# Performance work log

Measured on AMD Instinct MI355X. Metric: run time of the kernel, lower is better.

The kernel has to match this reference:

```python
import jax, jax.numpy as jnp
import numpy as np

HIDDEN = 1024
D_MEM = 256
BATCH = 4
SEQ = 1024
EPS = 1e-6


def elu_plus_one(x):
    # F.elu(x) + 1 == exp(x) for x<0, x+1 for x>=0 (positive feature map)
    return jnp.where(x > 0, x + 1.0, jnp.exp(x))


def setup_inputs() -> dict:
    key = jax.random.key(0)
    ks = jax.random.split(key, 8)
    hidden_states = jax.random.normal(ks[0], (BATCH, SEQ, HIDDEN), dtype=jnp.float32)
    s = 1.0 / np.sqrt(HIDDEN)
    w_q = jax.random.normal(ks[1], (D_MEM, HIDDEN), dtype=jnp.float32) * s
    w_k = jax.random.normal(ks[2], (D_MEM, HIDDEN), dtype=jnp.float32) * s
    w_v = jax.random.normal(ks[3], (D_MEM, HIDDEN), dtype=jnp.float32) * s
    w_o = jax.random.normal(ks[4], (HIDDEN, D_MEM), dtype=jnp.float32) * (1.0 / np.sqrt(D_MEM))
    gate = jnp.zeros((1,), dtype=jnp.float32)
    # nonzero persistent memory state so retrieval path is exercised
    memory = jax.random.normal(ks[5], (D_MEM, D_MEM), dtype=jnp.float32) * 0.1
    memory_norm = jax.random.uniform(ks[6], (D_MEM,), dtype=jnp.float32) * 10.0 + 1.0
    return {
        "hidden_states": hidden_states,
        "w_q": w_q, "w_k": w_k, "w_v": w_v, "w_o": w_o,
        "gate": gate, "memory": memory, "memory_norm": memory_norm,
    }


def _retrieve(sigma_x, memory, memory_norm):
    # [b,s,d] @ [d,d] -> [b,s,d], normalized by sigma_x @ memory_norm
    a_unnorm = jnp.matmul(sigma_x, memory)
    norm = jnp.clip(jnp.matmul(sigma_x, memory_norm), EPS, None)[..., None]
    out = a_unnorm / norm
    # torch: if memory_norm.sum() < 1e-6 -> zeros
    return jnp.where(memory_norm.sum() < EPS, jnp.zeros_like(out), out)


def reference(hidden_states, w_q, w_k, w_v, w_o, gate, memory, memory_norm):
    b, s, _ = hidden_states.shape
    q = jnp.einsum('bsh,dh->bsd', hidden_states, w_q)
    k = jnp.einsum('bsh,dh->bsd', hidden_states, w_k)
    v = jnp.einsum('bsh,dh->bsd', hidden_states, w_v)

    sigma_q = elu_plus_one(q)
    sigma_k = elu_plus_one(k)

    # --- retrieval from compressive memory ---
    memory_output = _retrieve(sigma_q, memory, memory_norm)

    # --- causal linear attention within segment (cumsum form, as in source) ---
    kv = jnp.einsum('bsd,bse->bsde', sigma_k, v)          # [b,s,d,d]
    kv_cumsum = jnp.cumsum(kv, axis=1)                     # [b,s,d,d]
    k_cumsum = jnp.cumsum(sigma_k, axis=1)                 # [b,s,d]
    numerator = jnp.einsum('bsd,bsde->bse', sigma_q, kv_cumsum)
    denominator = jnp.clip(jnp.einsum('bsd,bsd->bs', sigma_q, k_cumsum), EPS, None)[..., None]
    local_output = numerator / denominator

    g = jax.nn.sigmoid(gate[0])
    combined = g * memory_output + (1.0 - g) * local_output
    output = jnp.einsum('bsd,hd->bsh', combined, w_o)

    # --- delta-rule memory update (detached in torch) ---
    retrieved_unnorm = jnp.matmul(sigma_k, memory)
    norm = jnp.clip(jnp.matmul(sigma_k, memory_norm), EPS, None)[..., None]
    delta_v = v - retrieved_unnorm / norm
    memory_update = jnp.einsum('bsd,bse->de', sigma_k, delta_v) / (b * s)
    new_memory = jax.lax.stop_gradient(memory + memory_update)
    z_update = sigma_k.sum(axis=(0, 1)) / b
    new_memory_norm = jax.lax.stop_gradient(memory_norm + z_update)

    return output, new_memory, new_memory_norm
```

## Files before the change

kernel.cpp:

```cpp
#include <hip/hip_runtime.h>


#define HIDDEN 1024
#define DMEM 256
#define BATCH 4
#define SEQ 1024
#define MTOT (BATCH * SEQ)
#define CHUNK 128
#define NCH (SEQ / CHUNK)
#define NCHT (BATCH * NCH)
#define EPSF 1e-6f

typedef __bf16 bf16x8 __attribute__((ext_vector_type(8)));
typedef __bf16 bf16x4 __attribute__((ext_vector_type(4)));
typedef float f32x4 __attribute__((ext_vector_type(4)));

#define GL_LDS(g, l)                                                                   \
  __builtin_amdgcn_global_load_lds((const __attribute__((address_space(1))) void*)(g), \
                                   (__attribute__((address_space(3))) void*)(l), 16, 0, 0)

__device__ __forceinline__ float elu1(float x) { return x > 0.f ? x + 1.f : __expf(x); }

__global__ void kprep(const float* __restrict__ hs, const float* __restrict__ wq,
                      const float* __restrict__ wk, const float* __restrict__ wv,
                      const float* __restrict__ wo, const float* __restrict__ mem,
                      __bf16* __restrict__ hsb, __bf16* __restrict__ wqkvb,
                      __bf16* __restrict__ wob, __bf16* __restrict__ memT,
                      float* __restrict__ out) {
  __shared__ float s[64][65];
  int b = blockIdx.x, tid = threadIdx.x;
  if (b < 4096) {
    int i = b * 256 + tid;
    float4 f = reinterpret_cast<const float4*>(hs)[i];
    bf16x4 h = {(__bf16)f.x, (__bf16)f.y, (__bf16)f.z, (__bf16)f.w};
    reinterpret_cast<bf16x4*>(hsb)[i] = h;
  } else if (b < 5120) {
    int y = (b - 4096) >> 8;
    const float* src = (y == 0) ? wq : (y == 1) ? wk : (y == 2) ? wv : wo;
    __bf16* dst = (y < 3) ? wqkvb + (size_t)y * (DMEM * HIDDEN) : wob;
    int i = ((b - 4096) & 255) * 256 + tid;
    float4 f = reinterpret_cast<const float4*>(src)[i];
    bf16x4 h = {(__bf16)f.x, (__bf16)f.y, (__bf16)f.z, (__bf16)f.w};
    reinterpret_cast<bf16x4*>(dst)[i] = h;
  } else if (b < 5136) {
    int t = b - 5120;
    int bx = t & 3, by = t >> 2;
    int r0 = tid >> 6, col = tid & 63;
#pragma unroll
    for (int it = 0; it < 16; ++it) {
      int row = it * 4 + r0;
      s[row][col] = mem[(size_t)(by * 64 + row) * DMEM + bx * 64 + col];
    }
    __syncthreads();
#pragma unroll
    for (int it = 0; it < 16; ++it) {
      int row = it * 4 + r0;
      memT[(size_t)(bx * 64 + row) * DMEM + by * 64 + col] = (__bf16)s[col][row];
    }
  } else {
    int g = (b - 5136) * 256 + tid;
    reinterpret_cast<float4*>(out + (size_t)MTOT * HIDDEN)[g] =
        reinterpret_cast<const float4*>(mem)[g];
  }
}

__global__ __launch_bounds__(256) void k1_qkv_mfma(
    const __bf16* __restrict__ X, const __bf16* __restrict__ W, __bf16* __restrict__ sqb,
    __bf16* __restrict__ skb, __bf16* __restrict__ skT, __bf16* __restrict__ vT) {
  __shared__ __bf16 As[128 * 32];
  __shared__ __bf16 Bs[128 * 32];
  int tid = threadIdx.x;
  int lane = tid & 63, wave = tid >> 6;
  int m0 = blockIdx.x * 128;
  int by = blockIdx.y;
  int wsel = by >> 1, n0 = (by & 1) * 128;
  const __bf16* aptr = X + (size_t)(m0 + (tid >> 2)) * HIDDEN + ((tid & 3) << 3);
  const __bf16* bptr = W + (size_t)(by * 128 + (tid >> 2)) * HIDDEN + ((tid & 3) << 3);
  int wr = wave >> 1, wc = wave & 1, quad = lane >> 4, l16 = lane & 15;
  f32x4 acc[4][4] = {};
  for (int k0 = 0; k0 < HIDDEN; k0 += 32) {
    GL_LDS(aptr + k0, As + wave * 512);
    GL_LDS(aptr + (size_t)64 * HIDDEN + k0, As + 2048 + wave * 512);
    GL_LDS(bptr + k0, Bs + wave * 512);
    GL_LDS(bptr + (size_t)64 * HIDDEN + k0, Bs + 2048 + wave * 512);
    __syncthreads();
    bf16x8 aF[4], bF[4];
#pragma unroll
    for (int i = 0; i < 4; ++i)
      aF[i] = *reinterpret_cast<const bf16x8*>(As + (wr * 64 + i * 16 + l16) * 32 + quad * 8);
#pragma unroll
    for (int j = 0; j < 4; ++j)
      bF[j] = *reinterpret_cast<const bf16x8*>(Bs + (wc * 64 + j * 16 + l16) * 32 + quad * 8);
#pragma unroll
    for (int i = 0; i < 4; ++i)
#pragma unroll
      for (int j = 0; j < 4; ++j)
        acc[i][j] = __builtin_amdgcn_mfma_f32_16x16x32_bf16(aF[i], bF[j], acc[i][j], 0, 0, 0);
    __syncthreads();
  }
#pragma unroll
  for (int i = 0; i < 4; ++i)
#pragma unroll
    for (int j = 0; j < 4; ++j) {
      int mb = m0 + wr * 64 + i * 16 + quad * 4;
      int n = n0 + wc * 64 + j * 16 + l16;
      if (wsel == 0) {
#pragma unroll
        for (int r = 0; r < 4; ++r) sqb[(size_t)(mb + r) * DMEM + n] = (__bf16)elu1(acc[i][j][r]);
      } else if (wsel == 1) {
        bf16x4 t;
#pragma unroll
        for (int r = 0; r < 4; ++r) {
          float v = elu1(acc[i][j][r]);
          skb[(size_t)(mb + r) * DMEM + n] = (__bf16)v;
          t[r] = (__bf16)v;
        }
        *reinterpret_cast<bf16x4*>(skT + (size_t)n * MTOT + mb) = t;
      } else {
        bf16x4 t;
#pragma unroll
        for (int r = 0; r < 4; ++r) t[r] = (__bf16)acc[i][j][r];
        *reinterpret_cast<bf16x4*>(vT + (size_t)n * MTOT + mb) = t;
      }
    }
}

__global__ __launch_bounds__(256) void kC(const __bf16* __restrict__ vT,
                                          const __bf16* __restrict__ skT,
                                          const __bf16* __restrict__ sqb,
                                          const __bf16* __restrict__ skb,
                                          __bf16* __restrict__ kvcT, __bf16* __restrict__ scb,
                                          float* __restrict__ ksc) {
  __shared__ __bf16 As[64 * 32];
  __shared__ __bf16 Bs[128 * 32];
  int tid = threadIdx.x;
  int c = blockIdx.x;
  int y = blockIdx.y;
  if (y == 10) {
    int d = tid;
    float s = 0.f;
    for (int i = 0; i < CHUNK; ++i) s += (float)skb[(size_t)(c * CHUNK + i) * DMEM + d];
    ksc[c * DMEM + d] = s;
    return;
  }
  int lane = tid & 63, wave = tid >> 6;
  int wr = wave >> 1, wc = wave & 1, quad = lane >> 4, l16 = lane & 15;
  if (y < 8) {
    int e0 = (y >> 1) * 64, d0 = (y & 1) * 128;
    const __bf16* aptr = vT + (size_t)(e0 + (tid >> 2)) * MTOT + c * CHUNK + ((tid & 3) << 3);
    const __bf16* bptr = skT + (size_t)(d0 + (tid >> 2)) * MTOT + c * CHUNK + ((tid & 3) << 3);
    f32x4 acc[2][4] = {};
    for (int k0 = 0; k0 < CHUNK; k0 += 32) {
      GL_LDS(aptr + k0, As + wave * 512);
      GL_LDS(bptr + k0, Bs + wave * 512);
      GL_LDS(bptr + (size_t)64 * MTOT + k0, Bs + 2048 + wave * 512);
      __syncthreads();
      bf16x8 aF[2], bF[4];
#pragma unroll
      for (int i = 0; i < 2; ++i)
        aF[i] = *reinterpret_cast<const bf16x8*>(As + (wr * 32 + i * 16 + l16) * 32 + quad * 8);
#pragma unroll
      for (int j = 0; j < 4; ++j)
        bF[j] = *reinterpret_cast<const bf16x8*>(Bs + (wc * 64 + j * 16 + l16) * 32 + quad * 8);
#pragma unroll
      for (int i = 0; i < 2; ++i)
#pragma unroll
        for (int j = 0; j < 4; ++j)
          acc[i][j] = __builtin_amdgcn_mfma_f32_16x16x32_bf16(aF[i], bF[j], acc[i][j], 0, 0, 0);
      __syncthreads();
    }
#pragma unroll
    for (int i = 0; i < 2; ++i)
#pragma unroll
      for (int j = 0; j < 4; ++j)
#pragma unroll
        for (int r = 0; r < 4; ++r) {
          int e = e0 + wr * 32 + i * 16 + quad * 4 + r;
          int d = d0 + wc * 64 + j * 16 + l16;
          kvcT[(size_t)c * DMEM * DMEM + (size_t)e * DMEM + d] = (__bf16)acc[i][j][r];
        }
  } else {
    int i0 = (y - 8) * 64;
    const __bf16* aptr =
        sqb + (size_t)(c * CHUNK + i0 + (tid >> 2)) * DMEM + ((tid & 3) << 3);
    const __bf16* bptr = skb + (size_t)(c * CHUNK + (tid >> 2)) * DMEM + ((tid & 3) << 3);
    f32x4 acc[2][4] = {};
    for (int k0 = 0; k0 < DMEM; k0 += 32) {
      GL_LDS(aptr + k0, As + wave * 512);
      GL_LDS(bptr + k0, Bs + wave * 512);
      GL_LDS(bptr + (size_t)64 * DMEM + k0, Bs + 2048 + wave * 512);
      __syncthreads();
      bf16x8 aF[2], bF[4];
#pragma unroll
      for (int i = 0; i < 2; ++i)
        aF[i] = *reinterpret_cast<const bf16x8*>(As + (wr * 32 + i * 16 + l16) * 32 + quad * 8);
#pragma unroll
      for (int j = 0; j < 4; ++j)
        bF[j] = *reinterpret_cast<const bf16x8*>(Bs + (wc * 64 + j * 16 + l16) * 32 + quad * 8);
#pragma unroll
      for (int i = 0; i < 2; ++i)
#pragma unroll
        for (int j = 0; j < 4; ++j)
          acc[i][j] = __builtin_amdgcn_mfma_f32_16x16x32_bf16(aF[i], bF[j], acc[i][j], 0, 0, 0);
      __syncthreads();
    }
#pragma unroll
    for (int i = 0; i < 2; ++i)
#pragma unroll
      for (int j = 0; j < 4; ++j)
#pragma unroll
        for (int r = 0; r < 4; ++r) {
          int ii = i0 + wr * 32 + i * 16 + quad * 4 + r;
          int jj = wc * 64 + j * 16 + l16;
          scb[(size_t)c * CHUNK * CHUNK + (size_t)ii * CHUNK + jj] =
              (jj <= ii) ? (__bf16)acc[i][j][r] : (__bf16)0.f;
        }
  }
}

__global__ __launch_bounds__(256) void kD(const __bf16* __restrict__ kvcT,
                                          __bf16* __restrict__ kvpT,
                                          const float* __restrict__ ksc,
                                          const __bf16* __restrict__ scb,
                                          const __bf16* __restrict__ sqb,
                                          const __bf16* __restrict__ skb,
                                          const float* __restrict__ mnorm,
                                          float* __restrict__ den, float* __restrict__ qn,
                                          float* __restrict__ kn) {
  int vt = blockIdx.x;
  int tid = threadIdx.x;
  if (vt < 1024) {
    int batch = vt >> 8;
    int idx = (vt & 255) * 256 + tid;
    float run = 0.f;
    for (int c = 0; c < NCH; ++c) {
      size_t off = (size_t)(batch * NCH + c) * DMEM * DMEM + idx;
      kvpT[off] = (__bf16)run;
      run += (float)kvcT[off];
    }
  } else {
    int wave = tid >> 6, lane = tid & 63;
    int m = (vt - 1024) * 4 + wave;
    int c = m >> 7;
    int i = m & 127;
    int cb = c & ~7;
    float s_sc = 0.f, s_d2 = 0.f, s_qn = 0.f, s_kn = 0.f;
    for (int j = lane; j < CHUNK; j += 64)
      s_sc += (float)scb[(size_t)c * CHUNK * CHUNK + (size_t)i * CHUNK + j];
    for (int d = lane; d < DMEM; d += 64) {
      float q = (float)sqb[(size_t)m * DMEM + d];
      float k = (float)skb[(size_t)m * DMEM + d];
      float kp = 0.f;
      for (int cc = cb; cc < c; ++cc) kp += ksc[cc * DMEM + d];
      s_d2 += q * kp;
      s_qn += q * mnorm[d];
      s_kn += k * mnorm[d];
    }
#pragma unroll
    for (int off = 32; off > 0; off >>= 1) {
      s_sc += __shfl_down(s_sc, off);
      s_d2 += __shfl_down(s_d2, off);
      s_qn += __shfl_down(s_qn, off);
      s_kn += __shfl_down(s_kn, off);
    }
    if (lane == 0) {
      den[m] = s_sc + s_d2;
      qn[m] = s_qn;
      kn[m] = s_kn;
    }
  }
}

__global__ __launch_bounds__(256) void kE(const __bf16* __restrict__ scb,
                                          const __bf16* __restrict__ sqb,
                                          const __bf16* __restrict__ skb,
                                          const __bf16* __restrict__ vT,
                                          const __bf16* __restrict__ kvpT,
                                          const __bf16* __restrict__ memT,
                                          const float* __restrict__ den,
                                          const float* __restrict__ qn,
                                          const float* __restrict__ kn,
                                          const float* __restrict__ gate,
                                          const float* __restrict__ mnorm,
                                          __bf16* __restrict__ combb, __bf16* __restrict__ dvT) {
  __shared__ __bf16 As[128 * 32];
  __shared__ __bf16 B1s[128 * 32];
  __shared__ __bf16 B2s[128 * 32];
  __shared__ float flagsh;
  int tid = threadIdx.x;
  int lane = tid & 63, wave = tid >> 6;
  int wr = wave >> 1, wc = wave & 1, quad = lane >> 4, l16 = lane & 15;
  int bid = blockIdx.x;
  if (bid < 128) {
    if (tid == 0) {
      float s = 0.f;
      for (int d = 0; d < DMEM; ++d) s += mnorm[d];
      flagsh = (s < EPSF) ? 0.f : 1.f;
    }
    __syncthreads();
    float fl = flagsh;
    __syncthreads();
    int c = bid >> 2, yy = bid & 3;
    int i0 = (yy >> 1) * 64, e0 = (yy & 1) * 128;
    f32x4 acc_loc[2][4] = {};
    f32x4 acc_mem[2][4] = {};
    {
      const __bf16* aptr =
          scb + (size_t)c * CHUNK * CHUNK + (size_t)(i0 + (tid >> 2)) * CHUNK + ((tid & 3) << 3);
      const __bf16* bptr = vT + (size_t)(e0 + (tid >> 2)) * MTOT + c * CHUNK + ((tid & 3) << 3);
      for (int k0 = 0; k0 < CHUNK; k0 += 32) {
        GL_LDS(aptr + k0, As + wave * 512);
        GL_LDS(bptr + k0, B1s + wave * 512);
        GL_LDS(bptr + (size_t)64 * MTOT + k0, B1s + 2048 + wave * 512);
        __syncthreads();
        bf16x8 aF[2], bF[4];
#pragma unroll
        for (int i = 0; i < 2; ++i)
          aF[i] = *reinterpret_cast<const bf16x8*>(As + (wr * 32 + i * 16 + l16) * 32 + quad * 8);
#pragma unroll
        for (int j = 0; j < 4; ++j)
          bF[j] =
              *reinterpret_cast<const bf16x8*>(B1s + (wc * 64 + j * 16 + l16) * 32 + quad * 8);
#pragma unroll
        for (int i = 0; i < 2; ++i)
#pragma unroll
          for (int j = 0; j < 4; ++j)
            acc_loc[i][j] =
                __builtin_amdgcn_mfma_f32_16x16x32_bf16(aF[i], bF[j], acc_loc[i][j], 0, 0, 0);
        __syncthreads();
      }
    }
    {
      const __bf16* aptr =
          sqb + (size_t)(c * CHUNK + i0 + (tid >> 2)) * DMEM + ((tid & 3) << 3);
      const __bf16* b1ptr =
          kvpT + (size_t)c * DMEM * DMEM + (size_t)(e0 + (tid >> 2)) * DMEM + ((tid & 3) << 3);
      const __bf16* b2ptr = memT + (size_t)(e0 + (tid >> 2)) * DMEM + ((tid & 3) << 3);
      for (int k0 = 0; k0 < DMEM; k0 += 32) {
        GL_LDS(aptr + k0, As + wave * 512);
        GL_LDS(b1ptr + k0, B1s + wave * 512);
        GL_LDS(b1ptr + (size_t)64 * DMEM + k0, B1s + 2048 + wave * 512);
        GL_LDS(b2ptr + k0, B2s + wave * 512);
        GL_LDS(b2ptr + (size_t)64 * DMEM + k0, B2s + 2048 + wave * 512);
        __syncthreads();
        bf16x8 aF[2], b1F[4], b2F[4];
#pragma unroll
        for (int i = 0; i < 2; ++i)
          aF[i] = *reinterpret_cast<const bf16x8*>(As + (wr * 32 + i * 16 + l16) * 32 + quad * 8);
#pragma unroll
        for (int j = 0; j < 4; ++j) {
          b1F[j] =
              *reinterpret_cast<const bf16x8*>(B1s + (wc * 64 + j * 16 + l16) * 32 + quad * 8);
          b2F[j] =
              *reinterpret_cast<const bf16x8*>(B2s + (wc * 64 + j * 16 + l16) * 32 + quad * 8);
        }
#pragma unroll
        for (int i = 0; i < 2; ++i)
#pragma unroll
          for (int j = 0; j < 4; ++j) {
            acc_loc[i][j] =
                __builtin_amdgcn_mfma_f32_16x16x32_bf16(aF[i], b1F[j], acc_loc[i][j], 0, 0, 0);
            acc_mem[i][j] =
                __builtin_amdgcn_mfma_f32_16x16x32_bf16(aF[i], b2F[j], acc_mem[i][j], 0, 0, 0);
          }
        __syncthreads();
      }
    }
    float g = 1.f / (1.f + __expf(-gate[0]));
#pragma unroll
    for (int i = 0; i < 2; ++i) {
      int mb = c * CHUNK + i0 + wr * 32 + i * 16 + quad * 4;
      float dn[4], qv[4];
#pragma unroll
      for (int r = 0; r < 4; ++r) {
        dn[r] = fmaxf(den[mb + r], EPSF);
        qv[r] = fmaxf(qn[mb + r], EPSF);
      }
#pragma unroll
      for (int j = 0; j < 4; ++j) {
        int e = e0 + wc * 64 + j * 16 + l16;
#pragma unroll
        for (int r = 0; r < 4; ++r) {
          float comb = g * fl * acc_mem[i][j][r] / qv[r] + (1.f - g) * acc_loc[i][j][r] / dn[r];
          combb[(size_t)(mb + r) * DMEM + e] = (__bf16)comb;
        }
      }
    }
  } else {
    int t = bid - 128;
    int m0 = (t >> 1) * 128, n0 = (t & 1) * 128;
    const __bf16* aptr = skb + (size_t)(m0 + (tid >> 2)) * DMEM + ((tid & 3) << 3);
    const __bf16* bptr = memT + (size_t)(n0 + (tid >> 2)) * DMEM + ((tid & 3) << 3);
    f32x4 acc[4][4] = {};
    for (int k0 = 0; k0 < DMEM; k0 += 32) {
      GL_LDS(aptr + k0, As + wave * 512);
      GL_LDS(aptr + (size_t)64 * DMEM + k0, As + 2048 + wave * 512);
      GL_LDS(bptr + k0, B1s + wave * 512);
      GL_LDS(bptr + (size_t)64 * DMEM + k0, B1s + 2048 + wave * 512);
      __syncthreads();
      bf16x8 aF[4], bF[4];
#pragma unroll
      for (int i = 0; i < 4; ++i)
        aF[i] = *reinterpret_cast<const bf16x8*>(As + (wr * 64 + i * 16 + l16) * 32 + quad * 8);
#pragma unroll
      for (int j = 0; j < 4; ++j)
        bF[j] = *reinterpret_cast<const bf16x8*>(B1s + (wc * 64 + j * 16 + l16) * 32 + quad * 8);
#pragma unroll
      for (int i = 0; i < 4; ++i)
#pragma unroll
        for (int j = 0; j < 4; ++j)
          acc[i][j] = __builtin_amdgcn_mfma_f32_16x16x32_bf16(aF[i], bF[j], acc[i][j], 0, 0, 0);
      __syncthreads();
    }
#pragma unroll
    for (int i = 0; i < 4; ++i) {
      int mb = m0 + wr * 64 + i * 16 + quad * 4;
      float kv[4];
#pragma unroll
      for (int r = 0; r < 4; ++r) kv[r] = fmaxf(kn[mb + r], EPSF);
#pragma unroll
      for (int j = 0; j < 4; ++j) {
        int n = n0 + wc * 64 + j * 16 + l16;
        bf16x4 vv = *reinterpret_cast<const bf16x4*>(vT + (size_t)n * MTOT + mb);
        bf16x4 tt;
#pragma unroll
        for (int r = 0; r < 4; ++r) tt[r] = (__bf16)((float)vv[r] - acc[i][j][r] / kv[r]);
        *reinterpret_cast<bf16x4*>(dvT + (size_t)n * MTOT + mb) = tt;
      }
    }
  }
}

__global__ __launch_bounds__(256) void kF(const __bf16* __restrict__ combb,
                                          const __bf16* __restrict__ wob,
                                          const __bf16* __restrict__ skT,
                                          const __bf16* __restrict__ dvT,
                                          const float* __restrict__ ksc,
                                          const float* __restrict__ mnorm,
                                          float* __restrict__ out) {
  __shared__ __bf16 As[128 * 32];
  __shared__ __bf16 Bs[128 * 32];
  int tid = threadIdx.x;
  int bid = blockIdx.x;
  if (bid == 384) {
    int d = tid;
    float s = 0.f;
    for (int c = 0; c < NCHT; ++c) s += ksc[c * DMEM + d];
    out[(size_t)MTOT * HIDDEN + DMEM * DMEM + d] = mnorm[d] + s * (1.f / (float)BATCH);
    return;
  }
  int lane = tid & 63, wave = tid >> 6;
  int wr = wave >> 1, wc = wave & 1, quad = lane >> 4, l16 = lane & 15;
  if (bid < 256) {
    int m0 = (bid & 31) * 128, by = bid >> 5;
    const __bf16* aptr = combb + (size_t)(m0 + (tid >> 2)) * DMEM + ((tid & 3) << 3);
    const __bf16* bptr = wob + (size_t)(by * 128 + (tid >> 2)) * DMEM + ((tid & 3) << 3);
    f32x4 acc[4][4] = {};
    for (int k0 = 0; k0 < DMEM; k0 += 32) {
      GL_LDS(aptr + k0, As + wave * 512);
      GL_LDS(aptr + (size_t)64 * DMEM + k0, As + 2048 + wave * 512);
      GL_LDS(bptr + k0, Bs + wave * 512);
      GL_LDS(bptr + (size_t)64 * DMEM + k0, Bs + 2048 + wave * 512);
      __syncthreads();
      bf16x8 aF[4], bF[4];
#pragma unroll
      for (int i = 0; i < 4; ++i)
        aF[i] = *reinterpret_cast<const bf16x8*>(As + (wr * 64 + i * 16 + l16) * 32 + quad * 8);
#pragma unroll
      for (int j = 0; j < 4; ++j)
        bF[j] = *reinterpret_cast<const bf16x8*>(Bs + (wc * 64 + j * 16 + l16) * 32 + quad * 8);
#pragma unroll
      for (int i = 0; i < 4; ++i)
#pragma unroll
        for (int j = 0; j < 4; ++j)
          acc[i][j] = __builtin_amdgcn_mfma_f32_16x16x32_bf16(aF[i], bF[j], acc[i][j], 0, 0, 0);
      __syncthreads();
    }
#pragma unroll
    for (int i = 0; i < 4; ++i)
#pragma unroll
      for (int j = 0; j < 4; ++j)
#pragma unroll
        for (int r = 0; r < 4; ++r) {
          int m = m0 + wr * 64 + i * 16 + quad * 4 + r;
          int n = by * 128 + wc * 64 + j * 16 + l16;
          out[(size_t)m * HIDDEN + n] = acc[i][j][r];
        }
  } else {
    int t = bid - 256;
    int kbase = (t >> 3) * 256;
    int yy = t & 7;
    int d0 = (yy >> 1) * 64, e0 = (yy & 1) * 128;
    const __bf16* aptr = skT + (size_t)(d0 + (tid >> 2)) * MTOT + kbase + ((tid & 3) << 3);
    const __bf16* bptr = dvT + (size_t)(e0 + (tid >> 2)) * MTOT + kbase + ((tid & 3) << 3);
    f32x4 acc[2][4] = {};
    for (int k0 = 0; k0 < 256; k0 += 32) {
      GL_LDS(aptr + k0, As + wave * 512);
      GL_LDS(bptr + k0, Bs + wave * 512);
      GL_LDS(bptr + (size_t)64 * MTOT + k0, Bs + 2048 + wave * 512);
      __syncthreads();
      bf16x8 aF[2], bF[4];
#pragma unroll
      for (int i = 0; i < 2; ++i)
        aF[i] = *reinterpret_cast<const bf16x8*>(As + (wr * 32 + i * 16 + l16) * 32 + quad * 8);
#pragma unroll
      for (int j = 0; j < 4; ++j)
        bF[j] = *reinterpret_cast<const bf16x8*>(Bs + (wc * 64 + j * 16 + l16) * 32 + quad * 8);
#pragma unroll
      for (int i = 0; i < 2; ++i)
#pragma unroll
        for (int j = 0; j < 4; ++j)
          acc[i][j] = __builtin_amdgcn_mfma_f32_16x16x32_bf16(aF[i], bF[j], acc[i][j], 0, 0, 0);
      __syncthreads();
    }
    float* base = out + (size_t)MTOT * HIDDEN;
#pragma unroll
    for (int i = 0; i < 2; ++i)
#pragma unroll
      for (int j = 0; j < 4; ++j)
#pragma unroll
        for (int r = 0; r < 4; ++r) {
          int d = d0 + wr * 32 + i * 16 + quad * 4 + r;
          int e = e0 + wc * 64 + j * 16 + l16;
          atomicAdd(&base[(size_t)d * DMEM + e], acc[i][j][r] * (1.f / (float)MTOT));
        }
  }
}

extern "C" void kernel_launch(void* const* d_in, const int* in_sizes, int n_in,
                              void* d_out, int out_size, void* d_ws, size_t ws_size,
                              hipStream_t stream) {
  const float* hs = (const float*)d_in[0];
  const float* wq = (const float*)d_in[1];
  const float* wk = (const float*)d_in[2];
  const float* wv = (const float*)d_in[3];
  const float* wo = (const float*)d_in[4];
  const float* gate = (const float*)d_in[5];
  const float* mem = (const float*)d_in[6];
  const float* mnorm = (const float*)d_in[7];
  float* out = (float*)d_out;
  float* ws = (float*)d_ws;

  float* ksc = ws;
  float* den = ksc + 8192;
  float* qn = den + 4096;
  float* kn = qn + 4096;
  __bf16* kvcT = (__bf16*)(ws + 20480);
  __bf16* hsb = kvcT + (size_t)NCHT * DMEM * DMEM;
  __bf16* wqkvb = hsb + (size_t)MTOT * HIDDEN;
  __bf16* wob = wqkvb + (size_t)3 * DMEM * HIDDEN;
  __bf16* memT = wob + (size_t)HIDDEN * DMEM;
  __bf16* sqb = memT + (size_t)DMEM * DMEM;
  __bf16* skb = sqb + (size_t)MTOT * DMEM;
  __bf16* skT = skb + (size_t)MTOT * DMEM;
  __bf16* vT = skT + (size_t)MTOT * DMEM;
  __bf16* scb = vT + (size_t)MTOT * DMEM;
  __bf16* kvpT = scb + (size_t)NCHT * CHUNK * CHUNK;
  __bf16* combb = kvpT + (size_t)NCHT * DMEM * DMEM;
  __bf16* dvT = combb + (size_t)MTOT * DMEM;

  kprep<<<dim3(5200), 256, 0, stream>>>(hs, wq, wk, wv, wo, mem, hsb, wqkvb, wob, memT, out);
  k1_qkv_mfma<<<dim3(32, 6), 256, 0, stream>>>(hsb, wqkvb, sqb, skb, skT, vT);
  kC<<<dim3(NCHT, 11), 256, 0, stream>>>(vT, skT, sqb, skb, kvcT, scb, ksc);
  kD<<<dim3(2048), 256, 0, stream>>>(kvcT, kvpT, ksc, scb, sqb, skb, mnorm, den, qn, kn);
  kE<<<dim3(192), 256, 0, stream>>>(scb, sqb, skb, vT, kvpT, memT, den, qn, kn, gate, mnorm,
                                    combb, dvT);
  kF<<<dim3(385), 256, 0, stream>>>(combb, wob, skT, dvT, ksc, mnorm, out);
}
```

Before: 148.8 us.

## Use BK=64 shared GEMM helpers, larger tiles, vectorized scan, atomic-free memory update

```diff
diff --git a/kernel.cpp b/kernel.cpp
--- a/kernel.cpp
+++ b/kernel.cpp
@@ -21,12 +21,81 @@
 
 __device__ __forceinline__ float elu1(float x) { return x > 0.f ? x + 1.f : __expf(x); }
 
+__device__ __forceinline__ void stage128(const __bf16* p, long ld, int k0, __bf16* sm,
+                                         int wave) {
+  GL_LDS(p + k0, sm + wave * 512);
+  GL_LDS(p + (size_t)64 * ld + k0, sm + 2048 + wave * 512);
+  GL_LDS(p + k0 + 32, sm + 4096 + wave * 512);
+  GL_LDS(p + (size_t)64 * ld + k0 + 32, sm + 4096 + 2048 + wave * 512);
+}
+__device__ __forceinline__ void stage64(const __bf16* p, int k0, __bf16* sm, int wave) {
+  GL_LDS(p + k0, sm + wave * 512);
+  GL_LDS(p + k0 + 32, sm + 2048 + wave * 512);
+}
+
+__device__ __forceinline__ void gemm128_bk64(const __bf16* aptr, long lda, const __bf16* bptr,
+                                             long ldb, int klen, __bf16* smA, __bf16* smB,
+                                             int wave, int wr, int wc, int quad, int l16,
+                                             f32x4 (&acc)[4][4]) {
+  for (int k0 = 0; k0 < klen; k0 += 64) {
+    stage128(aptr, lda, k0, smA, wave);
+    stage128(bptr, ldb, k0, smB, wave);
+    __syncthreads();
+#pragma unroll
+    for (int h = 0; h < 2; ++h) {
+      bf16x8 aF[4], bF[4];
+#pragma unroll
+      for (int i = 0; i < 4; ++i)
+        aF[i] = *reinterpret_cast<const bf16x8*>(smA + h * 4096 +
+                                                 (wr * 64 + i * 16 + l16) * 32 + quad * 8);
+#pragma unroll
+      for (int j = 0; j < 4; ++j)
+        bF[j] = *reinterpret_cast<const bf16x8*>(smB + h * 4096 +
+                                                 (wc * 64 + j * 16 + l16) * 32 + quad * 8);
+#pragma unroll
+      for (int i = 0; i < 4; ++i)
+#pragma unroll
+        for (int j = 0; j < 4; ++j)
+          acc[i][j] = __builtin_amdgcn_mfma_f32_16x16x32_bf16(aF[i], bF[j], acc[i][j], 0, 0, 0);
+    }
+    __syncthreads();
+  }
+}
+
+__device__ __forceinline__ void gemm64_bk64(const __bf16* aptr, const __bf16* bptr, long ldb,
+                                            int klen, __bf16* smA, __bf16* smB, int wave,
+                                            int wr, int wc, int quad, int l16,
+                                            f32x4 (&acc)[2][4]) {
+  for (int k0 = 0; k0 < klen; k0 += 64) {
+    stage64(aptr, k0, smA, wave);
+    stage128(bptr, ldb, k0, smB, wave);
+    __syncthreads();
+#pragma unroll
+    for (int h = 0; h < 2; ++h) {
+      bf16x8 aF[2], bF[4];
+#pragma unroll
+      for (int i = 0; i < 2; ++i)
+        aF[i] = *reinterpret_cast<const bf16x8*>(smA + h * 2048 +
+                                                 (wr * 32 + i * 16 + l16) * 32 + quad * 8);
+#pragma unroll
+      for (int j = 0; j < 4; ++j)
+        bF[j] = *reinterpret_cast<const bf16x8*>(smB + h * 4096 +
+                                                 (wc * 64 + j * 16 + l16) * 32 + quad * 8);
+#pragma unroll
+      for (int i = 0; i < 2; ++i)
+#pragma unroll
+        for (int j = 0; j < 4; ++j)
+          acc[i][j] = __builtin_amdgcn_mfma_f32_16x16x32_bf16(aF[i], bF[j], acc[i][j], 0, 0, 0);
+    }
+    __syncthreads();
+  }
+}
+
 __global__ void kprep(const float* __restrict__ hs, const float* __restrict__ wq,
                       const float* __restrict__ wk, const float* __restrict__ wv,
                       const float* __restrict__ wo, const float* __restrict__ mem,
                       __bf16* __restrict__ hsb, __bf16* __restrict__ wqkvb,
-                      __bf16* __restrict__ wob, __bf16* __restrict__ memT,
-                      float* __restrict__ out) {
+                      __bf16* __restrict__ wob, __bf16* __restrict__ memT) {
   __shared__ float s[64][65];
   int b = blockIdx.x, tid = threadIdx.x;
   if (b < 4096) {
@@ -42,7 +111,7 @@
     float4 f = reinterpret_cast<const float4*>(src)[i];
     bf16x4 h = {(__bf16)f.x, (__bf16)f.y, (__bf16)f.z, (__bf16)f.w};
     reinterpret_cast<bf16x4*>(dst)[i] = h;
-  } else if (b < 5136) {
+  } else {
     int t = b - 5120;
     int bx = t & 3, by = t >> 2;
     int r0 = tid >> 6, col = tid & 63;
@@ -57,18 +126,14 @@
       int row = it * 4 + r0;
       memT[(size_t)(bx * 64 + row) * DMEM + by * 64 + col] = (__bf16)s[col][row];
     }
-  } else {
-    int g = (b - 5136) * 256 + tid;
-    reinterpret_cast<float4*>(out + (size_t)MTOT * HIDDEN)[g] =
-        reinterpret_cast<const float4*>(mem)[g];
   }
 }
 
 __global__ __launch_bounds__(256) void k1_qkv_mfma(
     const __bf16* __restrict__ X, const __bf16* __restrict__ W, __bf16* __restrict__ sqb,
     __bf16* __restrict__ skb, __bf16* __restrict__ skT, __bf16* __restrict__ vT) {
-  __shared__ __bf16 As[128 * 32];
-  __shared__ __bf16 Bs[128 * 32];
+  __shared__ __bf16 As[8192];
+  __shared__ __bf16 Bs[8192];
   int tid = threadIdx.x;
   int lane = tid & 63, wave = tid >> 6;
   int m0 = blockIdx.x * 128;
@@ -78,26 +143,7 @@
   const __bf16* bptr = W + (size_t)(by * 128 + (tid >> 2)) * HIDDEN + ((tid & 3) << 3);
   int wr = wave >> 1, wc = wave & 1, quad = lane >> 4, l16 = lane & 15;
   f32x4 acc[4][4] = {};
-  for (int k0 = 0; k0 < HIDDEN; k0 += 32) {
-    GL_LDS(aptr + k0, As + wave * 512);
-    GL_LDS(aptr + (size_t)64 * HIDDEN + k0, As + 2048 + wave * 512);
-    GL_LDS(bptr + k0, Bs + wave * 512);
-    GL_LDS(bptr + (size_t)64 * HIDDEN + k0, Bs + 2048 + wave * 512);
-    __syncthreads();
-    bf16x8 aF[4], bF[4];
-#pragma unroll
-    for (int i = 0; i < 4; ++i)
-      aF[i] = *reinterpret_cast<const bf16x8*>(As + (wr * 64 + i * 16 + l16) * 32 + quad * 8);
-#pragma unroll
-    for (int j = 0; j < 4; ++j)
-      bF[j] = *reinterpret_cast<const bf16x8*>(Bs + (wc * 64 + j * 16 + l16) * 32 + quad * 8);
-#pragma unroll
-    for (int i = 0; i < 4; ++i)
-#pragma unroll
-      for (int j = 0; j < 4; ++j)
-        acc[i][j] = __builtin_amdgcn_mfma_f32_16x16x32_bf16(aF[i], bF[j], acc[i][j], 0, 0, 0);
-    __syncthreads();
-  }
+  gemm128_bk64(aptr, HIDDEN, bptr, HIDDEN, HIDDEN, As, Bs, wave, wr, wc, quad, l16, acc);
 #pragma unroll
   for (int i = 0; i < 4; ++i)
 #pragma unroll
@@ -131,12 +177,12 @@
                                           const __bf16* __restrict__ skb,
                                           __bf16* __restrict__ kvcT, __bf16* __restrict__ scb,
                                           float* __restrict__ ksc) {
-  __shared__ __bf16 As[64 * 32];
-  __shared__ __bf16 Bs[128 * 32];
+  __shared__ __bf16 As[8192];
+  __shared__ __bf16 Bs[8192];
   int tid = threadIdx.x;
   int c = blockIdx.x;
   int y = blockIdx.y;
-  if (y == 10) {
+  if (y == 6) {
     int d = tid;
     float s = 0.f;
     for (int i = 0; i < CHUNK; ++i) s += (float)skb[(size_t)(c * CHUNK + i) * DMEM + d];
@@ -145,65 +191,28 @@
   }
   int lane = tid & 63, wave = tid >> 6;
   int wr = wave >> 1, wc = wave & 1, quad = lane >> 4, l16 = lane & 15;
-  if (y < 8) {
-    int e0 = (y >> 1) * 64, d0 = (y & 1) * 128;
+  if (y < 4) {
+    int e0 = (y >> 1) * 128, d0 = (y & 1) * 128;
     const __bf16* aptr = vT + (size_t)(e0 + (tid >> 2)) * MTOT + c * CHUNK + ((tid & 3) << 3);
     const __bf16* bptr = skT + (size_t)(d0 + (tid >> 2)) * MTOT + c * CHUNK + ((tid & 3) << 3);
-    f32x4 acc[2][4] = {};
-    for (int k0 = 0; k0 < CHUNK; k0 += 32) {
-      GL_LDS(aptr + k0, As + wave * 512);
-      GL_LDS(bptr + k0, Bs + wave * 512);
-      GL_LDS(bptr + (size_t)64 * MTOT + k0, Bs + 2048 + wave * 512);
-      __syncthreads();
-      bf16x8 aF[2], bF[4];
-#pragma unroll
-      for (int i = 0; i < 2; ++i)
-        aF[i] = *reinterpret_cast<const bf16x8*>(As + (wr * 32 + i * 16 + l16) * 32 + quad * 8);
+    f32x4 acc[4][4] = {};
+    gemm128_bk64(aptr, MTOT, bptr, MTOT, CHUNK, As, Bs, wave, wr, wc, quad, l16, acc);
+#pragma unroll
+    for (int i = 0; i < 4; ++i)
 #pragma unroll
       for (int j = 0; j < 4; ++j)
-        bF[j] = *reinterpret_cast<const bf16x8*>(Bs + (wc * 64 + j * 16 + l16) * 32 + quad * 8);
-#pragma unroll
-      for (int i = 0; i < 2; ++i)
-#pragma unroll
-        for (int j = 0; j < 4; ++j)
-          acc[i][j] = __builtin_amdgcn_mfma_f32_16x16x32_bf16(aF[i], bF[j], acc[i][j], 0, 0, 0);
-      __syncthreads();
-    }
-#pragma unroll
-    for (int i = 0; i < 2; ++i)
-#pragma unroll
-      for (int j = 0; j < 4; ++j)
 #pragma unroll
         for (int r = 0; r < 4; ++r) {
-          int e = e0 + wr * 32 + i * 16 + quad * 4 + r;
+          int e = e0 + wr * 64 + i * 16 + quad * 4 + r;
           int d = d0 + wc * 64 + j * 16 + l16;
           kvcT[(size_t)c * DMEM * DMEM + (size_t)e * DMEM + d] = (__bf16)acc[i][j][r];
         }
   } else {
-    int i0 = (y - 8) * 64;
-    const __bf16* aptr =
-        sqb + (size_t)(c * CHUNK + i0 + (tid >> 2)) * DMEM + ((tid & 3) << 3);
+    int i0 = (y - 4) * 64;
+    const __bf16* aptr = sqb + (size_t)(c * CHUNK + i0 + (tid >> 2)) * DMEM + ((tid & 3) << 3);
     const __bf16* bptr = skb + (size_t)(c * CHUNK + (tid >> 2)) * DMEM + ((tid & 3) << 3);
     f32x4 acc[2][4] = {};
-    for (int k0 = 0; k0 < DMEM; k0 += 32) {
-      GL_LDS(aptr + k0, As + wave * 512);
-      GL_LDS(bptr + k0, Bs + wave * 512);
-      GL_LDS(bptr + (size_t)64 * DMEM + k0, Bs + 2048 + wave * 512);
-      __syncthreads();
-      bf16x8 aF[2], bF[4];
-#pragma unroll
-      for (int i = 0; i < 2; ++i)
-        aF[i] = *reinterpret_cast<const bf16x8*>(As + (wr * 32 + i * 16 + l16) * 32 + quad * 8);
-#pragma unroll
-      for (int j = 0; j < 4; ++j)
-        bF[j] = *reinterpret_cast<const bf16x8*>(Bs + (wc * 64 + j * 16 + l16) * 32 + quad * 8);
-#pragma unroll
-      for (int i = 0; i < 2; ++i)
-#pragma unroll
-        for (int j = 0; j < 4; ++j)
-          acc[i][j] = __builtin_amdgcn_mfma_f32_16x16x32_bf16(aF[i], bF[j], acc[i][j], 0, 0, 0);
-      __syncthreads();
-    }
+    gemm64_bk64(aptr, bptr, DMEM, DMEM, As, Bs, wave, wr, wc, quad, l16, acc);
 #pragma unroll
     for (int i = 0; i < 2; ++i)
 #pragma unroll
@@ -229,18 +238,23 @@
                                           float* __restrict__ kn) {
   int vt = blockIdx.x;
   int tid = threadIdx.x;
-  if (vt < 1024) {
-    int batch = vt >> 8;
-    int idx = (vt & 255) * 256 + tid;
-    float run = 0.f;
+  if (vt < 128) {
+    int batch = vt >> 5;
+    size_t idx8 = (size_t)(((vt & 31) * 256 + tid)) * 8;
+    float run[8] = {};
     for (int c = 0; c < NCH; ++c) {
-      size_t off = (size_t)(batch * NCH + c) * DMEM * DMEM + idx;
-      kvpT[off] = (__bf16)run;
-      run += (float)kvcT[off];
+      size_t off = (size_t)(batch * NCH + c) * DMEM * DMEM + idx8;
+      bf16x8 t = *reinterpret_cast<const bf16x8*>(kvcT + off);
+      bf16x8 o;
+#pragma unroll
+      for (int r = 0; r < 8; ++r) o[r] = (__bf16)run[r];
+      *reinterpret_cast<bf16x8*>(kvpT + off) = o;
+#pragma unroll
+      for (int r = 0; r < 8; ++r) run[r] += (float)t[r];
     }
   } else {
     int wave = tid >> 6, lane = tid & 63;
-    int m = (vt - 1024) * 4 + wave;
+    int m = (vt - 128) * 4 + wave;
     int c = m >> 7;
     int i = m & 127;
     int cb = c & ~7;
@@ -283,9 +297,9 @@
                                           const float* __restrict__ gate,
                                           const float* __restrict__ mnorm,
                                           __bf16* __restrict__ combb, __bf16* __restrict__ dvT) {
-  __shared__ __bf16 As[128 * 32];
-  __shared__ __bf16 B1s[128 * 32];
-  __shared__ __bf16 B2s[128 * 32];
+  __shared__ __bf16 As[8192];
+  __shared__ __bf16 B1s[8192];
+  __shared__ __bf16 B2s[8192];
   __shared__ float flagsh;
   int tid = threadIdx.x;
   int lane = tid & 63, wave = tid >> 6;
@@ -308,61 +322,42 @@
       const __bf16* aptr =
           scb + (size_t)c * CHUNK * CHUNK + (size_t)(i0 + (tid >> 2)) * CHUNK + ((tid & 3) << 3);
       const __bf16* bptr = vT + (size_t)(e0 + (tid >> 2)) * MTOT + c * CHUNK + ((tid & 3) << 3);
-      for (int k0 = 0; k0 < CHUNK; k0 += 32) {
-        GL_LDS(aptr + k0, As + wave * 512);
-        GL_LDS(bptr + k0, B1s + wave * 512);
-        GL_LDS(bptr + (size_t)64 * MTOT + k0, B1s + 2048 + wave * 512);
-        __syncthreads();
-        bf16x8 aF[2], bF[4];
-#pragma unroll
-        for (int i = 0; i < 2; ++i)
-          aF[i] = *reinterpret_cast<const bf16x8*>(As + (wr * 32 + i * 16 + l16) * 32 + quad * 8);
-#pragma unroll
-        for (int j = 0; j < 4; ++j)
-          bF[j] =
-              *reinterpret_cast<const bf16x8*>(B1s + (wc * 64 + j * 16 + l16) * 32 + quad * 8);
-#pragma unroll
-        for (int i = 0; i < 2; ++i)
-#pragma unroll
-          for (int j = 0; j < 4; ++j)
-            acc_loc[i][j] =
-                __builtin_amdgcn_mfma_f32_16x16x32_bf16(aF[i], bF[j], acc_loc[i][j], 0, 0, 0);
-        __syncthreads();
-      }
+      gemm64_bk64(aptr, bptr, MTOT, CHUNK, As, B1s, wave, wr, wc, quad, l16, acc_loc);
     }
     {
-      const __bf16* aptr =
-          sqb + (size_t)(c * CHUNK + i0 + (tid >> 2)) * DMEM + ((tid & 3) << 3);
+      const __bf16* aptr = sqb + (size_t)(c * CHUNK + i0 + (tid >> 2)) * DMEM + ((tid & 3) << 3);
       const __bf16* b1ptr =
           kvpT + (size_t)c * DMEM * DMEM + (size_t)(e0 + (tid >> 2)) * DMEM + ((tid & 3) << 3);
       const __bf16* b2ptr = memT + (size_t)(e0 + (tid >> 2)) * DMEM + ((tid & 3) << 3);
-      for (int k0 = 0; k0 < DMEM; k0 += 32) {
-        GL_LDS(aptr + k0, As + wave * 512);
-        GL_LDS(b1ptr + k0, B1s + wave * 512);
-        GL_LDS(b1ptr + (size_t)64 * DMEM + k0, B1s + 2048 + wave * 512);
-        GL_LDS(b2ptr + k0, B2s + wave * 512);
-        GL_LDS(b2ptr + (size_t)64 * DMEM + k0, B2s + 2048 + wave * 512);
+      for (int k0 = 0; k0 < DMEM; k0 += 64) {
+        stage64(aptr, k0, As, wave);
+        stage128(b1ptr, DMEM, k0, B1s, wave);
+        stage128(b2ptr, DMEM, k0, B2s, wave);
         __syncthreads();
-        bf16x8 aF[2], b1F[4], b2F[4];
-#pragma unroll
-        for (int i = 0; i < 2; ++i)
-          aF[i] = *reinterpret_cast<const bf16x8*>(As + (wr * 32 + i * 16 + l16) * 32 + quad * 8);
-#pragma unroll
-        for (int j = 0; j < 4; ++j) {
-          b1F[j] =
-              *reinterpret_cast<const bf16x8*>(B1s + (wc * 64 + j * 16 + l16) * 32 + quad * 8);
-          b2F[j] =
-              *reinterpret_cast<const bf16x8*>(B2s + (wc * 64 + j * 16 + l16) * 32 + quad * 8);
-        }
-#pragma unroll
-        for (int i = 0; i < 2; ++i)
+#pragma unroll
+        for (int h = 0; h < 2; ++h) {
+          bf16x8 aF[2], b1F[4], b2F[4];
+#pragma unroll
+          for (int i = 0; i < 2; ++i)
+            aF[i] = *reinterpret_cast<const bf16x8*>(As + h * 2048 +
+                                                     (wr * 32 + i * 16 + l16) * 32 + quad * 8);
 #pragma unroll
           for (int j = 0; j < 4; ++j) {
-            acc_loc[i][j] =
-                __builtin_amdgcn_mfma_f32_16x16x32_bf16(aF[i], b1F[j], acc_loc[i][j], 0, 0, 0);
-            acc_mem[i][j] =
-                __builtin_amdgcn_mfma_f32_16x16x32_bf16(aF[i], b2F[j], acc_mem[i][j], 0, 0, 0);
+            b1F[j] = *reinterpret_cast<const bf16x8*>(B1s + h * 4096 +
+                                                      (wc * 64 + j * 16 + l16) * 32 + quad * 8);
+            b2F[j] = *reinterpret_cast<const bf16x8*>(B2s + h * 4096 +
+                                                      (wc * 64 + j * 16 + l16) * 32 + quad * 8);
           }
+#pragma unroll
+          for (int i = 0; i < 2; ++i)
+#pragma unroll
+            for (int j = 0; j < 4; ++j) {
+              acc_loc[i][j] =
+                  __builtin_amdgcn_mfma_f32_16x16x32_bf16(aF[i], b1F[j], acc_loc[i][j], 0, 0, 0);
+              acc_mem[i][j] =
+                  __builtin_amdgcn_mfma_f32_16x16x32_bf16(aF[i], b2F[j], acc_mem[i][j], 0, 0, 0);
+            }
+        }
         __syncthreads();
       }
     }
@@ -392,26 +387,7 @@
     const __bf16* aptr = skb + (size_t)(m0 + (tid >> 2)) * DMEM + ((tid & 3) << 3);
     const __bf16* bptr = memT + (size_t)(n0 + (tid >> 2)) * DMEM + ((tid & 3) << 3);
     f32x4 acc[4][4] = {};
-    for (int k0 = 0; k0 < DMEM; k0 += 32) {
-      GL_LDS(aptr + k0, As + wave * 512);
-      GL_LDS(aptr + (size_t)64 * DMEM + k0, As + 2048 + wave * 512);
-      GL_LDS(bptr + k0, B1s + wave * 512);
-      GL_LDS(bptr + (size_t)64 * DMEM + k0, B1s + 2048 + wave * 512);
-      __syncthreads();
-      bf16x8 aF[4], bF[4];
-#pragma unroll
-      for (int i = 0; i < 4; ++i)
-        aF[i] = *reinterpret_cast<const bf16x8*>(As + (wr * 64 + i * 16 + l16) * 32 + quad * 8);
-#pragma unroll
-      for (int j = 0; j < 4; ++j)
-        bF[j] = *reinterpret_cast<const bf16x8*>(B1s + (wc * 64 + j * 16 + l16) * 32 + quad * 8);
-#pragma unroll
-      for (int i = 0; i < 4; ++i)
-#pragma unroll
-        for (int j = 0; j < 4; ++j)
-          acc[i][j] = __builtin_amdgcn_mfma_f32_16x16x32_bf16(aF[i], bF[j], acc[i][j], 0, 0, 0);
-      __syncthreads();
-    }
+    gemm128_bk64(aptr, DMEM, bptr, DMEM, DMEM, As, B1s, wave, wr, wc, quad, l16, acc);
 #pragma unroll
     for (int i = 0; i < 4; ++i) {
       int mb = m0 + wr * 64 + i * 16 + quad * 4;
@@ -435,14 +411,15 @@
                                           const __bf16* __restrict__ wob,
                                           const __bf16* __restrict__ skT,
                                           const __bf16* __restrict__ dvT,
+                                          const float* __restrict__ mem,
                                           const float* __restrict__ ksc,
                                           const float* __restrict__ mnorm,
                                           float* __restrict__ out) {
-  __shared__ __bf16 As[128 * 32];
-  __shared__ __bf16 Bs[128 * 32];
+  __shared__ __bf16 As[8192];
+  __shared__ __bf16 Bs[8192];
   int tid = threadIdx.x;
   int bid = blockIdx.x;
-  if (bid == 384) {
+  if (bid == 260) {
     int d = tid;
     float s = 0.f;
     for (int c = 0; c < NCHT; ++c) s += ksc[c * DMEM + d];
@@ -456,26 +433,7 @@
     const __bf16* aptr = combb + (size_t)(m0 + (tid >> 2)) * DMEM + ((tid & 3) << 3);
     const __bf16* bptr = wob + (size_t)(by * 128 + (tid >> 2)) * DMEM + ((tid & 3) << 3);
     f32x4 acc[4][4] = {};
-    for (int k0 = 0; k0 < DMEM; k0 += 32) {
-      GL_LDS(aptr + k0, As + wave * 512);
-      GL_LDS(aptr + (size_t)64 * DMEM + k0, As + 2048 + wave * 512);
-      GL_LDS(bptr + k0, Bs + wave * 512);
-      GL_LDS(bptr + (size_t)64 * DMEM + k0, Bs + 2048 + wave * 512);
-      __syncthreads();
-      bf16x8 aF[4], bF[4];
-#pragma unroll
-      for (int i = 0; i < 4; ++i)
-        aF[i] = *reinterpret_cast<const bf16x8*>(As + (wr * 64 + i * 16 + l16) * 32 + quad * 8);
-#pragma unroll
-      for (int j = 0; j < 4; ++j)
-        bF[j] = *reinterpret_cast<const bf16x8*>(Bs + (wc * 64 + j * 16 + l16) * 32 + quad * 8);
-#pragma unroll
-      for (int i = 0; i < 4; ++i)
-#pragma unroll
-        for (int j = 0; j < 4; ++j)
-          acc[i][j] = __builtin_amdgcn_mfma_f32_16x16x32_bf16(aF[i], bF[j], acc[i][j], 0, 0, 0);
-      __syncthreads();
-    }
+    gemm128_bk64(aptr, DMEM, bptr, DMEM, DMEM, As, Bs, wave, wr, wc, quad, l16, acc);
 #pragma unroll
     for (int i = 0; i < 4; ++i)
 #pragma unroll
@@ -488,41 +446,22 @@
         }
   } else {
     int t = bid - 256;
-    int kbase = (t >> 3) * 256;
-    int yy = t & 7;
-    int d0 = (yy >> 1) * 64, e0 = (yy & 1) * 128;
-    const __bf16* aptr = skT + (size_t)(d0 + (tid >> 2)) * MTOT + kbase + ((tid & 3) << 3);
-    const __bf16* bptr = dvT + (size_t)(e0 + (tid >> 2)) * MTOT + kbase + ((tid & 3) << 3);
-    f32x4 acc[2][4] = {};
-    for (int k0 = 0; k0 < 256; k0 += 32) {
-      GL_LDS(aptr + k0, As + wave * 512);
-      GL_LDS(bptr + k0, Bs + wave * 512);
-      GL_LDS(bptr + (size_t)64 * MTOT + k0, Bs + 2048 + wave * 512);
-      __syncthreads();
-      bf16x8 aF[2], bF[4];
-#pragma unroll
-      for (int i = 0; i < 2; ++i)
-        aF[i] = *reinterpret_cast<const bf16x8*>(As + (wr * 32 + i * 16 + l16) * 32 + quad * 8);
+    int d0 = (t >> 1) * 128, e0 = (t & 1) * 128;
+    const __bf16* aptr = skT + (size_t)(d0 + (tid >> 2)) * MTOT + ((tid & 3) << 3);
+    const __bf16* bptr = dvT + (size_t)(e0 + (tid >> 2)) * MTOT + ((tid & 3) << 3);
+    f32x4 acc[4][4] = {};
+    gemm128_bk64(aptr, MTOT, bptr, MTOT, MTOT, As, Bs, wave, wr, wc, quad, l16, acc);
+    float* base = out + (size_t)MTOT * HIDDEN;
+#pragma unroll
+    for (int i = 0; i < 4; ++i)
 #pragma unroll
       for (int j = 0; j < 4; ++j)
-        bF[j] = *reinterpret_cast<const bf16x8*>(Bs + (wc * 64 + j * 16 + l16) * 32 + quad * 8);
-#pragma unroll
-      for (int i = 0; i < 2; ++i)
-#pragma unroll
-        for (int j = 0; j < 4; ++j)
-          acc[i][j] = __builtin_amdgcn_mfma_f32_16x16x32_bf16(aF[i], bF[j], acc[i][j], 0, 0, 0);
-      __syncthreads();
-    }
-    float* base = out + (size_t)MTOT * HIDDEN;
-#pragma unroll
-    for (int i = 0; i < 2; ++i)
-#pragma unroll
-      for (int j = 0; j < 4; ++j)
 #pragma unroll
         for (int r = 0; r < 4; ++r) {
-          int d = d0 + wr * 32 + i * 16 + quad * 4 + r;
+          int d = d0 + wr * 64 + i * 16 + quad * 4 + r;
           int e = e0 + wc * 64 + j * 16 + l16;
-          atomicAdd(&base[(size_t)d * DMEM + e], acc[i][j][r] * (1.f / (float)MTOT));
+          base[(size_t)d * DMEM + e] =
+              mem[(size_t)d * DMEM + e] + acc[i][j][r] * (1.f / (float)MTOT);
         }
   }
 }
@@ -559,11 +498,11 @@
   __bf16* combb = kvpT + (size_t)NCHT * DMEM * DMEM;
   __bf16* dvT = combb + (size_t)MTOT * DMEM;
 
-  kprep<<<dim3(5200), 256, 0, stream>>>(hs, wq, wk, wv, wo, mem, hsb, wqkvb, wob, memT, out);
+  kprep<<<dim3(5136), 256, 0, stream>>>(hs, wq, wk, wv, wo, mem, hsb, wqkvb, wob, memT);
   k1_qkv_mfma<<<dim3(32, 6), 256, 0, stream>>>(hsb, wqkvb, sqb, skb, skT, vT);
-  kC<<<dim3(NCHT, 11), 256, 0, stream>>>(vT, skT, sqb, skb, kvcT, scb, ksc);
-  kD<<<dim3(2048), 256, 0, stream>>>(kvcT, kvpT, ksc, scb, sqb, skb, mnorm, den, qn, kn);
+  kC<<<dim3(NCHT, 7), 256, 0, stream>>>(vT, skT, sqb, skb, kvcT, scb, ksc);
+  kD<<<dim3(1152), 256, 0, stream>>>(kvcT, kvpT, ksc, scb, sqb, skb, mnorm, den, qn, kn);
   kE<<<dim3(192), 256, 0, stream>>>(scb, sqb, skb, vT, kvpT, memT, den, qn, kn, gate, mnorm,
                                     combb, dvT);
-  kF<<<dim3(385), 256, 0, stream>>>(combb, wob, skT, dvT, ksc, mnorm, out);
-}
+  kF<<<dim3(261), 256, 0, stream>>>(combb, wob, skT, dvT, mem, ksc, mnorm, out);
+}
```

New measurement: 206.0 us. 38.4% more time.
